# Kernel tuning notes

Hardware: AMD Instinct MI355X
Metric: run time of the kernel (lower is better)

Reference implementation:

```python
import jax, jax.numpy as jnp
import numpy as np

N_NODES = 50000
N_EDGES = 320000
D_IN = 256
D_OUT = 256


def setup_inputs() -> dict:
    key = jax.random.key(0)
    k1, k2, k3, k4, k5, k6, k7 = jax.random.split(key, 7)
    s = 1.0 / np.sqrt(D_IN)
    return {
        "node_features": jax.random.normal(k1, (N_NODES, D_IN), dtype=jnp.float32),
        "edge_index": jax.random.randint(k2, (2, N_EDGES), 0, N_NODES, dtype=jnp.int64),
        "w1": jax.random.uniform(k3, (D_OUT, D_IN), jnp.float32, -s, s),
        "w2": jax.random.uniform(k4, (D_OUT, D_IN), jnp.float32, -s, s),
        "w3": jax.random.uniform(k5, (D_OUT, D_IN), jnp.float32, -s, s),
        "b3": jax.random.uniform(k6, (D_OUT,), jnp.float32, -s, s),
    }


def reference(node_features, edge_index, w1, w2, w3, b3):
    # GraphSAGE-style conv: project, gather messages from senders,
    # scatter-sum at receivers, project, combine with self term.
    n = node_features.shape[0]
    proj = node_features @ w3.T + b3                 # [N, D_OUT]
    msgs = proj[edge_index[0]]                       # [E, D_OUT] gather senders
    agg = jax.ops.segment_sum(msgs, edge_index[1], num_segments=n)  # [N, D_OUT]
    out = node_features @ w1.T + agg @ w2.T          # [N, D_OUT]
    return out
```

## Files before the change

kernel.cpp:

```cpp
#include <hip/hip_runtime.h>

#define NN 50000
#define NPAD 50048
#define NE 320000
#define D 256
#define CAP 64

typedef __bf16 bf16x8 __attribute__((ext_vector_type(8)));
typedef float f32x4 __attribute__((ext_vector_type(4)));

__device__ __forceinline__ unsigned short f2bf(float f) {
    unsigned u = __builtin_bit_cast(unsigned, f);
    unsigned r = u + 0x7FFFu + ((u >> 16) & 1u);
    return (unsigned short)(r >> 16);
}
__device__ __forceinline__ float bf2f(unsigned short h) {
    return __builtin_bit_cast(float, (unsigned)h << 16);
}

__global__ __launch_bounds__(256) void prep_weights(
        const float* __restrict__ w1, const float* __restrict__ w2,
        const float* __restrict__ w3, const float* __restrict__ b3,
        unsigned short* __restrict__ WTT, float* __restrict__ bvec) {
    const int j = blockIdx.x;
    const int k = threadIdx.x;
    __shared__ float w2row[D];
    __shared__ float red[D];
    w2row[k] = w2[j * D + k];
    __syncthreads();
    float acc = 0.f;
    #pragma unroll 8
    for (int o = 0; o < D; ++o) acc += w2row[o] * w3[o * D + k];
    WTT[(size_t)j * 512 + k]       = f2bf(w1[j * D + k]);
    WTT[(size_t)j * 512 + D + k]   = f2bf(acc);
    red[k] = w2row[k] * b3[k];
    __syncthreads();
    for (int s = 128; s > 0; s >>= 1) {
        if (k < s) red[k] += red[k + s];
        __syncthreads();
    }
    if (k == 0) bvec[j] = red[0];
}

__global__ __launch_bounds__(256) void convert_x(
        const float* __restrict__ x, unsigned short* __restrict__ xbf,
        int* __restrict__ cnt) {
    const size_t gid = (size_t)blockIdx.x * 256 + threadIdx.x;
    if (gid < NN) cnt[gid] = 0;
    const size_t i = gid * 8;
    if (i >= (size_t)NN * D) return;
    const float4 a = *reinterpret_cast<const float4*>(x + i);
    const float4 b = *reinterpret_cast<const float4*>(x + i + 4);
    ushort4 o0 = {f2bf(a.x), f2bf(a.y), f2bf(a.z), f2bf(a.w)};
    ushort4 o1 = {f2bf(b.x), f2bf(b.y), f2bf(b.z), f2bf(b.w)};
    *reinterpret_cast<ushort4*>(xbf + i)     = o0;
    *reinterpret_cast<ushort4*>(xbf + i + 4) = o1;
}

__global__ __launch_bounds__(256) void fill_csr(
        const int* __restrict__ ei, int* __restrict__ csr, int* __restrict__ cnt) {
    const int e = blockIdx.x * 256 + threadIdx.x;
    if (e >= NE) return;
    const int src = ei[e];
    const int dst = ei[NE + e];
    const int pos = atomicAdd(cnt + dst, 1);
    if (pos < CAP) csr[(size_t)dst * CAP + pos] = src;
}

__global__ __launch_bounds__(256) void agg_gather(
        const unsigned short* __restrict__ xbf, const int* __restrict__ csr,
        const int* __restrict__ cnt, unsigned short* __restrict__ aggbf) {
    const int node = blockIdx.x * 4 + (threadIdx.x >> 6);
    const int lane = threadIdx.x & 63;
    if (node >= NN) return;
    int d = cnt[node]; if (d > CAP) d = CAP;
    const int* __restrict__ row = csr + (size_t)node * CAP;
    float a0 = 0.f, a1 = 0.f, a2 = 0.f, a3 = 0.f;
    int i = 0;
    for (; i + 2 <= d; i += 2) {
        const ushort4 v0 = *reinterpret_cast<const ushort4*>(xbf + (size_t)row[i] * D + lane * 4);
        const ushort4 v1 = *reinterpret_cast<const ushort4*>(xbf + (size_t)row[i + 1] * D + lane * 4);
        a0 += bf2f(v0.x) + bf2f(v1.x); a1 += bf2f(v0.y) + bf2f(v1.y);
        a2 += bf2f(v0.z) + bf2f(v1.z); a3 += bf2f(v0.w) + bf2f(v1.w);
    }
    if (i < d) {
        const ushort4 v = *reinterpret_cast<const ushort4*>(xbf + (size_t)row[i] * D + lane * 4);
        a0 += bf2f(v.x); a1 += bf2f(v.y); a2 += bf2f(v.z); a3 += bf2f(v.w);
    }
    ushort4 o = {f2bf(a0), f2bf(a1), f2bf(a2), f2bf(a3)};
    *reinterpret_cast<ushort4*>(aggbf + (size_t)node * D + lane * 4) = o;
}

__global__ __launch_bounds__(256) void gemm_mfma(
        const unsigned short* __restrict__ xbf, const unsigned short* __restrict__ aggbf,
        const unsigned short* __restrict__ WTT, const float* __restrict__ bvec,
        const int* __restrict__ cnt, float* __restrict__ out) {
    __shared__ __align__(16) unsigned short ldsA[2][128 * 64];
    __shared__ __align__(16) unsigned short ldsB[2][128 * 64];

    const int tid  = threadIdx.x;
    const int w    = tid >> 6;
    const int lane = tid & 63;
    const int wm   = w >> 1, wn = w & 1;
    const int mb   = blockIdx.x >> 1;
    const int nb0  = (blockIdx.x & 1) * 128;
    const int gr0  = mb * 128;

    auto stage = [&](int kt, int b) {
        const unsigned short* __restrict__ srcA = (kt < 4) ? xbf : aggbf;
        const int kcA = (kt & 3) * 64;
        const int kcB = kt * 64;
        #pragma unroll
        for (int p = 0; p < 4; ++p) {
            const int idx = p * 256 + w * 64 + lane;
            const int r = idx >> 3, c = idx & 7;
            const int sw = (c ^ (r & 7)) << 3;
            const unsigned short* gpA = srcA + ((size_t)(gr0 + r) << 8) + kcA + sw;
            unsigned short* lpA = &ldsA[b][(p * 256 + w * 64) << 3];
            __builtin_amdgcn_global_load_lds(
                (const __attribute__((address_space(1))) void*)(const void*)gpA,
                (__attribute__((address_space(3))) void*)(void*)lpA, 16, 0, 0);
            const unsigned short* gpB = WTT + ((size_t)(nb0 + r) << 9) + kcB + sw;
            unsigned short* lpB = &ldsB[b][(p * 256 + w * 64) << 3];
            __builtin_amdgcn_global_load_lds(
                (const __attribute__((address_space(1))) void*)(const void*)gpB,
                (__attribute__((address_space(3))) void*)(void*)lpB, 16, 0, 0);
        }
    };

    f32x4 acc[4][4];
    #pragma unroll
    for (int a = 0; a < 4; ++a)
        #pragma unroll
        for (int b = 0; b < 4; ++b) acc[a][b] = (f32x4)0.f;

    stage(0, 0);
    __syncthreads();
    #pragma unroll 2
    for (int kt = 0; kt < 8; ++kt) {
        const int cur = kt & 1;
        if (kt < 7) stage(kt + 1, cur ^ 1);
        #pragma unroll
        for (int kh = 0; kh < 2; ++kh) {
            const int cbase = kh * 4 + (lane >> 4);
            bf16x8 af[4], bfr[4];
            #pragma unroll
            for (int f = 0; f < 4; ++f) {
                const int ra = wm * 64 + f * 16 + (lane & 15);
                af[f] = *reinterpret_cast<const bf16x8*>(
                    &ldsA[cur][ra * 64 + ((cbase ^ (ra & 7)) << 3)]);
                const int rb = wn * 64 + f * 16 + (lane & 15);
                bfr[f] = *reinterpret_cast<const bf16x8*>(
                    &ldsB[cur][rb * 64 + ((cbase ^ (rb & 7)) << 3)]);
            }
            #pragma unroll
            for (int fm = 0; fm < 4; ++fm)
                #pragma unroll
                for (int fn = 0; fn < 4; ++fn)
                    acc[fm][fn] = __builtin_amdgcn_mfma_f32_16x16x32_bf16(
                        af[fm], bfr[fn], acc[fm][fn], 0, 0, 0);
        }
        __syncthreads();
    }

    const int col0 = nb0 + wn * 64 + (lane & 15);
    float bv[4];
    #pragma unroll
    for (int fn = 0; fn < 4; ++fn) bv[fn] = bvec[col0 + fn * 16];
    #pragma unroll
    for (int fm = 0; fm < 4; ++fm) {
        #pragma unroll
        for (int i = 0; i < 4; ++i) {
            const int row = gr0 + wm * 64 + fm * 16 + ((lane >> 4) << 2) + i;
            if (row < NN) {
                const float dg = (float)cnt[row];
                float* op = out + ((size_t)row << 8) + col0;
                #pragma unroll
                for (int fn = 0; fn < 4; ++fn)
                    op[fn * 16] = acc[fm][fn][i] + dg * bv[fn];
            }
        }
    }
}

extern "C" void kernel_launch(void* const* d_in, const int* in_sizes, int n_in,
                              void* d_out, int out_size, void* d_ws, size_t ws_size,
                              hipStream_t stream) {
    const float* x  = (const float*)d_in[0];
    const int*   ei = (const int*)d_in[1];
    const float* w1 = (const float*)d_in[2];
    const float* w2 = (const float*)d_in[3];
    const float* w3 = (const float*)d_in[4];
    const float* b3 = (const float*)d_in[5];
    float* out = (float*)d_out;

    unsigned short* xbf   = (unsigned short*)d_ws;
    unsigned short* aggbf = xbf + (size_t)NPAD * D;
    unsigned short* WTT   = aggbf + (size_t)NPAD * D;
    float* bvec = (float*)(WTT + (size_t)D * 512);
    int*   cnt  = (int*)(bvec + D);
    int*   csr  = cnt + NN;

    prep_weights<<<D, 256, 0, stream>>>(w1, w2, w3, b3, WTT, bvec);
    convert_x<<<(NN * D) / (256 * 8), 256, 0, stream>>>(x, xbf, cnt);
    fill_csr<<<(NE + 255) / 256, 256, 0, stream>>>(ei, csr, cnt);
    agg_gather<<<(NN + 3) / 4, 256, 0, stream>>>(xbf, csr, cnt, aggbf);
    gemm_mfma<<<((NN + 127) / 128) * 2, 256, 0, stream>>>(xbf, aggbf, WTT, bvec, cnt, out);
}
```

Measured before the change: 112.0 us.

## Fuse neighbor aggregation into GEMM kernel with LDS-resident aggregate tile

Removes the separate gather kernel and the aggbf round trip through global memory. Each 64-row block first gathers and sums neighbor features into a swizzled LDS tile, then runs both GEMM halves. The x and weight fragments are now read straight from global memory instead of through double-buffered LDS staging, and each block covers all 256 output columns. This saves a launch and the aggregate write/read, at the cost of losing the async LDS pipelining and coalesced staging for the GEMM operands.

New measurement: 136.6 us. 22.0% more time.

```diff
diff --git a/kernel.cpp b/kernel.cpp
--- a/kernel.cpp
+++ b/kernel.cpp
@@ -16,6 +16,15 @@
 }
 __device__ __forceinline__ float bf2f(unsigned short h) {
     return __builtin_bit_cast(float, (unsigned)h << 16);
+}
+__device__ __forceinline__ float bflo(unsigned u) {
+    return __builtin_bit_cast(float, u << 16);
+}
+__device__ __forceinline__ float bfhi(unsigned u) {
+    return __builtin_bit_cast(float, u & 0xFFFF0000u);
+}
+__device__ __forceinline__ unsigned packbf(float lo, float hi) {
+    return (unsigned)f2bf(lo) | ((unsigned)f2bf(hi) << 16);
 }
 
 __global__ __launch_bounds__(256) void prep_weights(
@@ -67,66 +76,70 @@
     if (pos < CAP) csr[(size_t)dst * CAP + pos] = src;
 }
 
-__global__ __launch_bounds__(256) void agg_gather(
-        const unsigned short* __restrict__ xbf, const int* __restrict__ csr,
-        const int* __restrict__ cnt, unsigned short* __restrict__ aggbf) {
-    const int node = blockIdx.x * 4 + (threadIdx.x >> 6);
-    const int lane = threadIdx.x & 63;
-    if (node >= NN) return;
-    int d = cnt[node]; if (d > CAP) d = CAP;
-    const int* __restrict__ row = csr + (size_t)node * CAP;
-    float a0 = 0.f, a1 = 0.f, a2 = 0.f, a3 = 0.f;
-    int i = 0;
-    for (; i + 2 <= d; i += 2) {
-        const ushort4 v0 = *reinterpret_cast<const ushort4*>(xbf + (size_t)row[i] * D + lane * 4);
-        const ushort4 v1 = *reinterpret_cast<const ushort4*>(xbf + (size_t)row[i + 1] * D + lane * 4);
-        a0 += bf2f(v0.x) + bf2f(v1.x); a1 += bf2f(v0.y) + bf2f(v1.y);
-        a2 += bf2f(v0.z) + bf2f(v1.z); a3 += bf2f(v0.w) + bf2f(v1.w);
-    }
-    if (i < d) {
-        const ushort4 v = *reinterpret_cast<const ushort4*>(xbf + (size_t)row[i] * D + lane * 4);
-        a0 += bf2f(v.x); a1 += bf2f(v.y); a2 += bf2f(v.z); a3 += bf2f(v.w);
-    }
-    ushort4 o = {f2bf(a0), f2bf(a1), f2bf(a2), f2bf(a3)};
-    *reinterpret_cast<ushort4*>(aggbf + (size_t)node * D + lane * 4) = o;
-}
-
-__global__ __launch_bounds__(256) void gemm_mfma(
-        const unsigned short* __restrict__ xbf, const unsigned short* __restrict__ aggbf,
-        const unsigned short* __restrict__ WTT, const float* __restrict__ bvec,
-        const int* __restrict__ cnt, float* __restrict__ out) {
-    __shared__ __align__(16) unsigned short ldsA[2][128 * 64];
-    __shared__ __align__(16) unsigned short ldsB[2][128 * 64];
+__global__ __launch_bounds__(256) void gemm_fused(
+        const unsigned short* __restrict__ xbf, const unsigned short* __restrict__ WTT,
+        const float* __restrict__ bvec, const int* __restrict__ cnt,
+        const int* __restrict__ csr, float* __restrict__ out) {
+    __shared__ __align__(16) unsigned short aggL[64 * 256];
 
     const int tid  = threadIdx.x;
     const int w    = tid >> 6;
     const int lane = tid & 63;
-    const int wm   = w >> 1, wn = w & 1;
-    const int mb   = blockIdx.x >> 1;
-    const int nb0  = (blockIdx.x & 1) * 128;
-    const int gr0  = mb * 128;
-
-    auto stage = [&](int kt, int b) {
-        const unsigned short* __restrict__ srcA = (kt < 4) ? xbf : aggbf;
-        const int kcA = (kt & 3) * 64;
-        const int kcB = kt * 64;
-        #pragma unroll
-        for (int p = 0; p < 4; ++p) {
-            const int idx = p * 256 + w * 64 + lane;
-            const int r = idx >> 3, c = idx & 7;
-            const int sw = (c ^ (r & 7)) << 3;
-            const unsigned short* gpA = srcA + ((size_t)(gr0 + r) << 8) + kcA + sw;
-            unsigned short* lpA = &ldsA[b][(p * 256 + w * 64) << 3];
-            __builtin_amdgcn_global_load_lds(
-                (const __attribute__((address_space(1))) void*)(const void*)gpA,
-                (__attribute__((address_space(3))) void*)(void*)lpA, 16, 0, 0);
-            const unsigned short* gpB = WTT + ((size_t)(nb0 + r) << 9) + kcB + sw;
-            unsigned short* lpB = &ldsB[b][(p * 256 + w * 64) << 3];
-            __builtin_amdgcn_global_load_lds(
-                (const __attribute__((address_space(1))) void*)(const void*)gpB,
-                (__attribute__((address_space(3))) void*)(void*)lpB, 16, 0, 0);
-        }
-    };
+    const int gr0  = blockIdx.x * 64;
+
+    {
+        const int sub = lane >> 4;
+        const int l16 = lane & 15;
+        #pragma unroll
+        for (int pass = 0; pass < 4; ++pass) {
+            const int r  = w * 16 + pass * 4 + sub;
+            const int gr = gr0 + r;
+            int d = 0;
+            if (gr < NN) { d = cnt[gr]; if (d > CAP) d = CAP; }
+            const int* __restrict__ row = csr + (size_t)gr * CAP;
+            float a[16];
+            #pragma unroll
+            for (int j = 0; j < 16; ++j) a[j] = 0.f;
+            int i = 0;
+            for (; i + 2 <= d; i += 2) {
+                const int s0 = row[i], s1 = row[i + 1];
+                const uint4 p0 = *reinterpret_cast<const uint4*>(xbf + (size_t)s0 * D + l16 * 8);
+                const uint4 p1 = *reinterpret_cast<const uint4*>(xbf + (size_t)s0 * D + 128 + l16 * 8);
+                const uint4 q0 = *reinterpret_cast<const uint4*>(xbf + (size_t)s1 * D + l16 * 8);
+                const uint4 q1 = *reinterpret_cast<const uint4*>(xbf + (size_t)s1 * D + 128 + l16 * 8);
+                a[0] += bflo(p0.x) + bflo(q0.x); a[1] += bfhi(p0.x) + bfhi(q0.x);
+                a[2] += bflo(p0.y) + bflo(q0.y); a[3] += bfhi(p0.y) + bfhi(q0.y);
+                a[4] += bflo(p0.z) + bflo(q0.z); a[5] += bfhi(p0.z) + bfhi(q0.z);
+                a[6] += bflo(p0.w) + bflo(q0.w); a[7] += bfhi(p0.w) + bfhi(q0.w);
+                a[8]  += bflo(p1.x) + bflo(q1.x); a[9]  += bfhi(p1.x) + bfhi(q1.x);
+                a[10] += bflo(p1.y) + bflo(q1.y); a[11] += bfhi(p1.y) + bfhi(q1.y);
+                a[12] += bflo(p1.z) + bflo(q1.z); a[13] += bfhi(p1.z) + bfhi(q1.z);
+                a[14] += bflo(p1.w) + bflo(q1.w); a[15] += bfhi(p1.w) + bfhi(q1.w);
+            }
+            if (i < d) {
+                const int s0 = row[i];
+                const uint4 p0 = *reinterpret_cast<const uint4*>(xbf + (size_t)s0 * D + l16 * 8);
+                const uint4 p1 = *reinterpret_cast<const uint4*>(xbf + (size_t)s0 * D + 128 + l16 * 8);
+                a[0] += bflo(p0.x); a[1] += bfhi(p0.x);
+                a[2] += bflo(p0.y); a[3] += bfhi(p0.y);
+                a[4] += bflo(p0.z); a[5] += bfhi(p0.z);
+                a[6] += bflo(p0.w); a[7] += bfhi(p0.w);
+                a[8]  += bflo(p1.x); a[9]  += bfhi(p1.x);
+                a[10] += bflo(p1.y); a[11] += bfhi(p1.y);
+                a[12] += bflo(p1.z); a[13] += bfhi(p1.z);
+                a[14] += bflo(p1.w); a[15] += bfhi(p1.w);
+            }
+            uint4 o0 = {packbf(a[0], a[1]),  packbf(a[2], a[3]),
+                        packbf(a[4], a[5]),  packbf(a[6], a[7])};
+            uint4 o1 = {packbf(a[8], a[9]),  packbf(a[10], a[11]),
+                        packbf(a[12], a[13]), packbf(a[14], a[15])};
+            const int u0 = l16 ^ (r & 7);
+            const int u1 = (16 + l16) ^ (r & 7);
+            *reinterpret_cast<uint4*>(&aggL[(r * 32 + u0) * 8]) = o0;
+            *reinterpret_cast<uint4*>(&aggL[(r * 32 + u1) * 8]) = o1;
+        }
+    }
+    __syncthreads();
 
     f32x4 acc[4][4];
     #pragma unroll
@@ -134,24 +147,21 @@
         #pragma unroll
         for (int b = 0; b < 4; ++b) acc[a][b] = (f32x4)0.f;
 
-    stage(0, 0);
-    __syncthreads();
-    #pragma unroll 2
-    for (int kt = 0; kt < 8; ++kt) {
-        const int cur = kt & 1;
-        if (kt < 7) stage(kt + 1, cur ^ 1);
+    const int l16g = lane & 15;
+    const int g4   = lane >> 4;
+
+    #pragma unroll
+    for (int kt = 0; kt < 4; ++kt) {
         #pragma unroll
         for (int kh = 0; kh < 2; ++kh) {
-            const int cbase = kh * 4 + (lane >> 4);
+            const int ko = kt * 64 + kh * 32 + g4 * 8;
             bf16x8 af[4], bfr[4];
             #pragma unroll
             for (int f = 0; f < 4; ++f) {
-                const int ra = wm * 64 + f * 16 + (lane & 15);
-                af[f] = *reinterpret_cast<const bf16x8*>(
-                    &ldsA[cur][ra * 64 + ((cbase ^ (ra & 7)) << 3)]);
-                const int rb = wn * 64 + f * 16 + (lane & 15);
-                bfr[f] = *reinterpret_cast<const bf16x8*>(
-                    &ldsB[cur][rb * 64 + ((cbase ^ (rb & 7)) << 3)]);
+                const int ra = gr0 + f * 16 + l16g;
+                af[f] = *reinterpret_cast<const bf16x8*>(xbf + ((size_t)ra << 8) + ko);
+                const int rb = w * 64 + f * 16 + l16g;
+                bfr[f] = *reinterpret_cast<const bf16x8*>(WTT + ((size_t)rb << 9) + ko);
             }
             #pragma unroll
             for (int fm = 0; fm < 4; ++fm)
@@ -160,10 +170,32 @@
                     acc[fm][fn] = __builtin_amdgcn_mfma_f32_16x16x32_bf16(
                         af[fm], bfr[fn], acc[fm][fn], 0, 0, 0);
         }
-        __syncthreads();
-    }
-
-    const int col0 = nb0 + wn * 64 + (lane & 15);
+    }
+    #pragma unroll
+    for (int kt = 0; kt < 4; ++kt) {
+        #pragma unroll
+        for (int kh = 0; kh < 2; ++kh) {
+            const int cb = kt * 8 + kh * 4 + g4;
+            bf16x8 af[4], bfr[4];
+            #pragma unroll
+            for (int f = 0; f < 4; ++f) {
+                const int r = f * 16 + l16g;
+                af[f] = *reinterpret_cast<const bf16x8*>(
+                    &aggL[(r * 32 + (cb ^ (r & 7))) * 8]);
+                const int rb = w * 64 + f * 16 + l16g;
+                bfr[f] = *reinterpret_cast<const bf16x8*>(
+                    WTT + ((size_t)rb << 9) + 256 + cb * 8);
+            }
+            #pragma unroll
+            for (int fm = 0; fm < 4; ++fm)
+                #pragma unroll
+                for (int fn = 0; fn < 4; ++fn)
+                    acc[fm][fn] = __builtin_amdgcn_mfma_f32_16x16x32_bf16(
+                        af[fm], bfr[fn], acc[fm][fn], 0, 0, 0);
+        }
+    }
+
+    const int col0 = w * 64 + l16g;
     float bv[4];
     #pragma unroll
     for (int fn = 0; fn < 4; ++fn) bv[fn] = bvec[col0 + fn * 16];
@@ -171,7 +203,7 @@
     for (int fm = 0; fm < 4; ++fm) {
         #pragma unroll
         for (int i = 0; i < 4; ++i) {
-            const int row = gr0 + wm * 64 + fm * 16 + ((lane >> 4) << 2) + i;
+            const int row = gr0 + fm * 16 + g4 * 4 + i;
             if (row < NN) {
                 const float dg = (float)cnt[row];
                 float* op = out + ((size_t)row << 8) + col0;
@@ -194,9 +226,8 @@
     const float* b3 = (const float*)d_in[5];
     float* out = (float*)d_out;
 
-    unsigned short* xbf   = (unsigned short*)d_ws;
-    unsigned short* aggbf = xbf + (size_t)NPAD * D;
-    unsigned short* WTT   = aggbf + (size_t)NPAD * D;
+    unsigned short* xbf = (unsigned short*)d_ws;
+    unsigned short* WTT = xbf + (size_t)NPAD * D;
     float* bvec = (float*)(WTT + (size_t)D * 512);
     int*   cnt  = (int*)(bvec + D);
     int*   csr  = cnt + NN;
@@ -204,6 +235,5 @@
     prep_weights<<<D, 256, 0, stream>>>(w1, w2, w3, b3, WTT, bvec);
     convert_x<<<(NN * D) / (256 * 8), 256, 0, stream>>>(x, xbf, cnt);
     fill_csr<<<(NE + 255) / 256, 256, 0, stream>>>(ei, csr, cnt);
-    agg_gather<<<(NN + 3) / 4, 256, 0, stream>>>(xbf, csr, cnt, aggbf);
-    gemm_mfma<<<((NN + 127) / 128) * 2, 256, 0, stream>>>(xbf, aggbf, WTT, bvec, cnt, out);
-}
+    gemm_fused<<<NPAD / 64, 256, 0, stream>>>(xbf, WTT, bvec, cnt, csr, out);
+}
```
